# Kernel optimization log

Measured on AMD Instinct MI355X. Metric: run time of the kernel, lower is better.

## Reference

```python
import jax, jax.numpy as jnp
import numpy as np

DIM = 512
NUM_HEADS = 1
WS = 16
B, H, W = 2, WS * WS, 1


def _rel_pos_index(ws):
    # matches Attention.calculate_relative_position_index (no Swin offset -> negatives)
    coords = np.stack(np.meshgrid(np.arange(ws), np.arange(ws), indexing='ij'), 0).reshape(2, -1)
    rel = coords[:, :, None] - coords[:, None, :]          # [2, ws^2, ws^2]
    return rel.transpose(1, 2, 0).sum(-1)                  # [ws^2, ws^2] in [-(2ws-2), 2ws-2]

_NTAB = (2 * WS - 1) ** 2
# torch fancy indexing wraps negative indices; emulate with mod (values are in (-NTAB, NTAB))
_RPI = np.mod(_rel_pos_index(WS), _NTAB).reshape(-1)       # [ws^4]


def setup_inputs() -> dict:
    key = jax.random.key(0)
    ks = jax.random.split(key, 6)
    x = jax.random.normal(ks[0], (B, DIM, H, W), dtype=jnp.float32)
    qkv_w = jax.random.normal(ks[1], (3 * DIM, DIM), dtype=jnp.float32) * (DIM ** -0.5)
    qkv_b = jax.random.normal(ks[2], (3 * DIM,), dtype=jnp.float32) * 0.02
    proj_w = jax.random.normal(ks[3], (DIM, DIM), dtype=jnp.float32) * (DIM ** -0.5)
    proj_b = jax.random.normal(ks[4], (DIM,), dtype=jnp.float32) * 0.02
    rpb = jax.random.normal(ks[5], (_NTAB, NUM_HEADS), dtype=jnp.float32) * 0.02
    return {"x": x, "qkv_w": qkv_w, "qkv_b": qkv_b,
            "proj_w": proj_w, "proj_b": proj_b, "rpb": rpb}


def reference(x, qkv_w, qkv_b, proj_w, proj_b, rpb):
    b, c, h, w = x.shape                                   # [B, C, H, W=1]
    d = c // NUM_HEADS
    scale = d ** -0.5                                      # qk_scale=None -> (dim//nh)^-0.5
    # 1x1 conv == channel matmul
    qkv = jnp.einsum('bchw,oc->bohw', x, qkv_w) + qkv_b[None, :, None, None]
    qkv = qkv.reshape(b, 3, NUM_HEADS, d, h, w)
    q, k, v = qkv[:, 0], qkv[:, 1], qkv[:, 2]              # [B, nh, d, H, W]
    # matmul over last two dims: contracts W -> [B, nh, d, H, H]
    attn = jnp.einsum('bndhw,bndgw->bndhg', q, k) * scale
    idx = jnp.asarray(_RPI)
    bias = rpb[idx].reshape(h * w, h * w, -1).transpose(2, 0, 1)  # [nh, HW, HW] = [1, H, H]
    attn = jax.nn.softmax(attn + bias, axis=-1)
    out = jnp.einsum('bndhg,bndgw->bndhw', attn, v).sum(axis=1)   # sum over heads -> [B, d, H, W]
    out = jnp.einsum('bchw,oc->bohw', out, proj_w) + proj_b[None, :, None, None]
    return out
```

## Files before the change

### kernel.cpp

```cpp
#include <hip/hip_runtime.h>


#define TOK    256
#define KDIM   512
#define K8     64
#define LOG2E  1.4426950408889634f
#define SCALE  0.04419417382415922f

#define OFF_WQAH 0
#define OFF_WQAL 786432
#define OFF_XBH  1572864
#define OFF_XBL  1835008
#define OFF_WPAH 2097152
#define OFF_WPAL 2359296
#define OFF_AOBH 2621440
#define OFF_AOBL 2883584
#define OFF_QKVF 1572864

#define EXP2(x) __builtin_amdgcn_exp2f(x)

typedef __attribute__((ext_vector_type(8))) short short8_t;
typedef __attribute__((ext_vector_type(4))) float f32x4;

__device__ __forceinline__ unsigned short f2bf(float x) {
    unsigned int u = __float_as_uint(x);
    u += 0x7fffu + ((u >> 16) & 1u);
    return (unsigned short)(u >> 16);
}
__device__ __forceinline__ float bf2f(unsigned short h) {
    return __uint_as_float((unsigned int)h << 16);
}

__device__ __forceinline__ void cvt8(const float* v, unsigned short* hq,
                                     unsigned short* lq) {
#pragma unroll
    for (int j = 0; j < 8; ++j) {
        const unsigned short h = f2bf(v[j]);
        hq[j] = h;
        lq[j] = f2bf(v[j] - bf2f(h));
    }
}

__global__ __launch_bounds__(256)
void prep(const float* __restrict__ qkv_w, const float* __restrict__ x,
          const float* __restrict__ proj_w, unsigned short* __restrict__ U)
{
    const int id = blockIdx.x * 256 + threadIdx.x;
    alignas(16) unsigned short hq[8], lq[8];
    float v[8];

    if (id < 98304) {
        const int m = id >> 6, kc = id & 63;
        const float* s = qkv_w + (size_t)m * KDIM + kc * 8;
#pragma unroll
        for (int j = 0; j < 8; ++j) v[j] = s[j];
        cvt8(v, hq, lq);
        const size_t o = ((size_t)(m >> 4) * K8 + kc) * 128 + (size_t)(m & 15) * 8;
        *(uint4*)(U + OFF_WQAH + o) = *(const uint4*)hq;
        *(uint4*)(U + OFF_WQAL + o) = *(const uint4*)lq;
    } else if (id < 131072) {
        const int rid = id - 98304;
        const int n = rid & 255, kc = (rid >> 8) & 63, b = rid >> 14;
        const float* s = x + ((size_t)b * KDIM + kc * 8) * TOK + n;
#pragma unroll
        for (int j = 0; j < 8; ++j) v[j] = s[(size_t)j * TOK];
        cvt8(v, hq, lq);
        const size_t o = (((size_t)b * 16 + (n >> 4)) * K8 + kc) * 128
                         + (size_t)(n & 15) * 8;
        *(uint4*)(U + OFF_XBH + o) = *(const uint4*)hq;
        *(uint4*)(U + OFF_XBL + o) = *(const uint4*)lq;
    } else if (id < 163840) {
        const int rid = id - 131072;
        const int m = rid >> 6, kc = rid & 63;
        const float* s = proj_w + (size_t)m * KDIM + kc * 8;
#pragma unroll
        for (int j = 0; j < 8; ++j) v[j] = s[j];
        cvt8(v, hq, lq);
        const size_t o = ((size_t)(m >> 4) * K8 + kc) * 128 + (size_t)(m & 15) * 8;
        *(uint4*)(U + OFF_WPAH + o) = *(const uint4*)hq;
        *(uint4*)(U + OFF_WPAL + o) = *(const uint4*)lq;
    }
}

template<bool BIAS>
__global__ __launch_bounds__(64)
void gemm_frag(const unsigned short* __restrict__ Ah,
               const unsigned short* __restrict__ Al,
               const unsigned short* __restrict__ Bh,
               const unsigned short* __restrict__ Bl,
               const float* __restrict__ bias,
               float* __restrict__ Cout, int Mtot)
{
    const int t   = threadIdx.x;
    const int lr  = t & 15;
    const int lg  = t >> 4;
    const int mt0 = blockIdx.x * 2;
    const int nt0 = blockIdx.y * 4;
    const int b   = blockIdx.z;

    f32x4 acc[2][4];
#pragma unroll
    for (int mi = 0; mi < 2; ++mi)
#pragma unroll
        for (int ni = 0; ni < 4; ++ni)
            acc[mi][ni] = (f32x4){0.f, 0.f, 0.f, 0.f};

    short8_t ah[2][2], al[2][2], bh[2][4], bl[2][4];

#define LDF(S, P) do {                                                        \
        const int kc_ = (S) * 4 + lg;                                         \
        _Pragma("unroll")                                                     \
        for (int mi = 0; mi < 2; ++mi) {                                      \
            const size_t o_ = ((size_t)(mt0 + mi) * K8 + kc_) * 128           \
                              + (size_t)lr * 8;                               \
            ah[P][mi] = *(const short8_t*)(Ah + o_);                          \
            al[P][mi] = *(const short8_t*)(Al + o_);                          \
        }                                                                     \
        _Pragma("unroll")                                                     \
        for (int ni = 0; ni < 4; ++ni) {                                      \
            const size_t o_ = (((size_t)b * 16 + nt0 + ni) * K8 + kc_) * 128  \
                              + (size_t)lr * 8;                               \
            bh[P][ni] = *(const short8_t*)(Bh + o_);                          \
            bl[P][ni] = *(const short8_t*)(Bl + o_);                          \
        }                                                                     \
    } while (0)

    LDF(0, 0);
#pragma unroll
    for (int s = 0; s < 16; ++s) {
        const int p = s & 1;
        if (s + 1 < 16) LDF(s + 1, p ^ 1);
#pragma unroll
        for (int mi = 0; mi < 2; ++mi)
#pragma unroll
            for (int ni = 0; ni < 4; ++ni) {
                acc[mi][ni] = __builtin_amdgcn_mfma_f32_16x16x32_bf16(
                    ah[p][mi], bh[p][ni], acc[mi][ni], 0, 0, 0);
                acc[mi][ni] = __builtin_amdgcn_mfma_f32_16x16x32_bf16(
                    al[p][mi], bh[p][ni], acc[mi][ni], 0, 0, 0);
                acc[mi][ni] = __builtin_amdgcn_mfma_f32_16x16x32_bf16(
                    ah[p][mi], bl[p][ni], acc[mi][ni], 0, 0, 0);
            }
    }
#undef LDF

#pragma unroll
    for (int mi = 0; mi < 2; ++mi)
#pragma unroll
        for (int r = 0; r < 4; ++r) {
            const int row = (mt0 + mi) * 16 + lg * 4 + r;
            const float pb = BIAS ? bias[row] : 0.f;
#pragma unroll
            for (int ni = 0; ni < 4; ++ni) {
                const int col = (nt0 + ni) * 16 + lr;
                Cout[((size_t)b * Mtot + row) * TOK + col] = acc[mi][ni][r] + pb;
            }
        }
}

__global__ __launch_bounds__(256)
void attn_f32(const float* __restrict__ qkvf, const float* __restrict__ qkv_b,
              const float* __restrict__ rpb,
              unsigned short* __restrict__ aoh, unsigned short* __restrict__ aol)
{
    __shared__ float ks_[2][TOK];
    __shared__ float vs_[2][TOK];
    __shared__ float tab2[64];
    __shared__ float brow[31][258];
    __shared__ float lpart[2][TOK];
    __shared__ float apart[2][TOK];

    const int t  = threadIdx.x;
    const int b  = blockIdx.y;
    const int d0 = blockIdx.x * 2;
    const float* q0 = qkvf + (size_t)b * (1536 * TOK);

    if (t < 61) {
        const int rel = t - 30;
        tab2[t] = rpb[rel < 0 ? rel + 961 : rel] * LOG2E;
    }
    {
        const int sel = t >> 7;
        const int row = (t >> 6) & 1;
        const int g4  = (t & 63) * 4;
        const int o   = (sel ? 1024 : 512) + d0 + row;
        const float bb = qkv_b[o];
        float4 v = *(const float4*)(q0 + (size_t)o * TOK + g4);
        v.x += bb; v.y += bb; v.z += bb; v.w += bb;
        if (sel == 0) {
            const float s = SCALE * LOG2E;
            v.x *= s; v.y *= s; v.z *= s; v.w *= s;
            *(float4*)&ks_[row][g4] = v;
        } else {
            *(float4*)&vs_[row][g4] = v;
        }
    }
    __syncthreads();
    {
        const int rg = ((t >> 4) & 15) + (t & 15);
#pragma unroll 1
        for (int it = 0; it < 31; ++it)
            brow[it][t] = tab2[it - rg + 30];
    }
    __syncthreads();

    const int w   = t >> 6;
    const int dl  = w & 1;
    const int gh  = w >> 1;
    const int hl  = t & 63;
    const int qi  = ((hl & 15) << 2) | (hl >> 4);
    const int h0  = qi * 4;
    const int rh0 = (qi >> 2) + 4 * (qi & 3);

    float q[4];
    {
        const float bb = qkv_b[d0 + dl];
        const float4 x4 = *(const float4*)(q0 + (size_t)(d0 + dl) * TOK + h0);
        q[0] = x4.x + bb; q[1] = x4.y + bb; q[2] = x4.z + bb; q[3] = x4.w + bb;
    }

    float l[4]  = {0.f, 0.f, 0.f, 0.f};
    float am[4] = {0.f, 0.f, 0.f, 0.f};

    const int pbeg = gh * 128;
#pragma unroll 2
    for (int p = pbeg; p < pbeg + 128; p += 4) {
        const float4 k4 = *(const float4*)&ks_[dl][p];
        const float4 v4 = *(const float4*)&vs_[dl][p];
#pragma unroll
        for (int r = 0; r < 4; ++r) {
            const float2 b01 = *(const float2*)&brow[rh0 + r][p];
            const float2 b23 = *(const float2*)&brow[rh0 + r][p + 2];
            float e;
            e = EXP2(fmaf(q[r], k4.x, b01.x)); l[r] += e; am[r] = fmaf(e, v4.x, am[r]);
            e = EXP2(fmaf(q[r], k4.y, b01.y)); l[r] += e; am[r] = fmaf(e, v4.y, am[r]);
            e = EXP2(fmaf(q[r], k4.z, b23.x)); l[r] += e; am[r] = fmaf(e, v4.z, am[r]);
            e = EXP2(fmaf(q[r], k4.w, b23.y)); l[r] += e; am[r] = fmaf(e, v4.w, am[r]);
        }
    }

    if (gh == 1) {
        *(float4*)&lpart[dl][h0] = make_float4(l[0], l[1], l[2], l[3]);
        *(float4*)&apart[dl][h0] = make_float4(am[0], am[1], am[2], am[3]);
    }
    __syncthreads();
    if (gh == 0) {
        const float4 lo = *(const float4*)&lpart[dl][h0];
        const float4 ao = *(const float4*)&apart[dl][h0];
        float vals[4];
        vals[0] = (am[0] + ao.x) / (l[0] + lo.x);
        vals[1] = (am[1] + ao.y) / (l[1] + lo.y);
        vals[2] = (am[2] + ao.z) / (l[2] + lo.z);
        vals[3] = (am[3] + ao.w) / (l[3] + lo.w);
        const int d = d0 + dl;
        const size_t ob = (((size_t)b * 16 + (h0 >> 4)) * K8 + (d >> 3)) * 128
                          + (size_t)(h0 & 15) * 8 + (d & 7);
#pragma unroll
        for (int r = 0; r < 4; ++r) {
            const unsigned short hh = f2bf(vals[r]);
            aoh[ob + (size_t)r * 8] = hh;
            aol[ob + (size_t)r * 8] = f2bf(vals[r] - bf2f(hh));
        }
    }
}

extern "C" void kernel_launch(void* const* d_in, const int* in_sizes, int n_in,
                              void* d_out, int out_size, void* d_ws, size_t ws_size,
                              hipStream_t stream)
{
    const float* x      = (const float*)d_in[0];
    const float* qkv_w  = (const float*)d_in[1];
    const float* qkv_b  = (const float*)d_in[2];
    const float* proj_w = (const float*)d_in[3];
    const float* proj_b = (const float*)d_in[4];
    const float* rpb    = (const float*)d_in[5];
    float* out = (float*)d_out;

    unsigned short* U = (unsigned short*)d_ws;
    float* qkvf = (float*)d_ws + OFF_QKVF;

    prep<<<dim3(640), 256, 0, stream>>>(qkv_w, x, proj_w, U);

    gemm_frag<false><<<dim3(48, 4, 2), 64, 0, stream>>>(
        U + OFF_WQAH, U + OFF_WQAL, U + OFF_XBH, U + OFF_XBL,
        nullptr, qkvf, 1536);

    attn_f32<<<dim3(256, 2), 256, 0, stream>>>(qkvf, qkv_b, rpb,
                                               U + OFF_AOBH, U + OFF_AOBL);

    gemm_frag<true><<<dim3(16, 4, 2), 64, 0, stream>>>(
        U + OFF_WPAH, U + OFF_WPAL, U + OFF_AOBH, U + OFF_AOBL,
        proj_b, out, 512);
}
```

Measured before the change: 116.0 us.

## Split GEMM K-dimension across four waves with shared-memory reduction

Each GEMM block now runs four wavefronts that each handle a quarter of the K dimension. Their partial accumulators are summed through shared memory and written out as coalesced float4 stores. The projection GEMM also uses one M-tile per block, which doubles its block count. The goal is to shorten each wave's serial MFMA chain and give the small GEMMs more parallelism, at the cost of extra LDS traffic and a block-wide barrier.

```diff
diff --git a/kernel.cpp b/kernel.cpp
--- a/kernel.cpp
+++ b/kernel.cpp
@@ -82,8 +82,8 @@
     }
 }
 
-template<bool BIAS>
-__global__ __launch_bounds__(64)
+template<int MT, bool BIAS>
+__global__ __launch_bounds__(256)
 void gemm_frag(const unsigned short* __restrict__ Ah,
                const unsigned short* __restrict__ Al,
                const unsigned short* __restrict__ Bh,
@@ -91,26 +91,30 @@
                const float* __restrict__ bias,
                float* __restrict__ Cout, int Mtot)
 {
-    const int t   = threadIdx.x;
-    const int lr  = t & 15;
-    const int lg  = t >> 4;
-    const int mt0 = blockIdx.x * 2;
-    const int nt0 = blockIdx.y * 4;
-    const int b   = blockIdx.z;
-
-    f32x4 acc[2][4];
-#pragma unroll
-    for (int mi = 0; mi < 2; ++mi)
+    alignas(16) __shared__ float red[4][MT * 16][68];
+
+    const int t    = threadIdx.x;
+    const int w    = t >> 6;
+    const int lane = t & 63;
+    const int lr   = lane & 15;
+    const int lg   = lane >> 4;
+    const int mt0  = blockIdx.x * MT;
+    const int nt0  = blockIdx.y * 4;
+    const int b    = blockIdx.z;
+
+    f32x4 acc[MT][4];
+#pragma unroll
+    for (int mi = 0; mi < MT; ++mi)
 #pragma unroll
         for (int ni = 0; ni < 4; ++ni)
             acc[mi][ni] = (f32x4){0.f, 0.f, 0.f, 0.f};
 
-    short8_t ah[2][2], al[2][2], bh[2][4], bl[2][4];
+    short8_t ah[2][MT], al[2][MT], bh[2][4], bl[2][4];
 
 #define LDF(S, P) do {                                                        \
-        const int kc_ = (S) * 4 + lg;                                         \
+        const int kc_ = w * 16 + (S) * 4 + lg;                                \
         _Pragma("unroll")                                                     \
-        for (int mi = 0; mi < 2; ++mi) {                                      \
+        for (int mi = 0; mi < MT; ++mi) {                                     \
             const size_t o_ = ((size_t)(mt0 + mi) * K8 + kc_) * 128           \
                               + (size_t)lr * 8;                               \
             ah[P][mi] = *(const short8_t*)(Ah + o_);                          \
@@ -127,11 +131,11 @@
 
     LDF(0, 0);
 #pragma unroll
-    for (int s = 0; s < 16; ++s) {
+    for (int s = 0; s < 4; ++s) {
         const int p = s & 1;
-        if (s + 1 < 16) LDF(s + 1, p ^ 1);
-#pragma unroll
-        for (int mi = 0; mi < 2; ++mi)
+        if (s + 1 < 4) LDF(s + 1, p ^ 1);
+#pragma unroll
+        for (int mi = 0; mi < MT; ++mi)
 #pragma unroll
             for (int ni = 0; ni < 4; ++ni) {
                 acc[mi][ni] = __builtin_amdgcn_mfma_f32_16x16x32_bf16(
@@ -145,17 +149,33 @@
 #undef LDF
 
 #pragma unroll
-    for (int mi = 0; mi < 2; ++mi)
-#pragma unroll
-        for (int r = 0; r < 4; ++r) {
-            const int row = (mt0 + mi) * 16 + lg * 4 + r;
-            const float pb = BIAS ? bias[row] : 0.f;
-#pragma unroll
-            for (int ni = 0; ni < 4; ++ni) {
-                const int col = (nt0 + ni) * 16 + lr;
-                Cout[((size_t)b * Mtot + row) * TOK + col] = acc[mi][ni][r] + pb;
-            }
+    for (int mi = 0; mi < MT; ++mi)
+#pragma unroll
+        for (int ni = 0; ni < 4; ++ni)
+#pragma unroll
+            for (int r = 0; r < 4; ++r)
+                red[w][mi * 16 + lg * 4 + r][ni * 16 + lr] = acc[mi][ni][r];
+    __syncthreads();
+
+#pragma unroll
+    for (int it = 0; it < MT; ++it) {
+        const int rr = it * 16 + (t >> 4);
+        const int cc = (t & 15) * 4;
+        float4 v0 = *(const float4*)&red[0][rr][cc];
+        const float4 v1 = *(const float4*)&red[1][rr][cc];
+        const float4 v2 = *(const float4*)&red[2][rr][cc];
+        const float4 v3 = *(const float4*)&red[3][rr][cc];
+        v0.x += v1.x + v2.x + v3.x;
+        v0.y += v1.y + v2.y + v3.y;
+        v0.z += v1.z + v2.z + v3.z;
+        v0.w += v1.w + v2.w + v3.w;
+        const int grow = mt0 * 16 + rr;
+        if (BIAS) {
+            const float pb = bias[grow];
+            v0.x += pb; v0.y += pb; v0.z += pb; v0.w += pb;
         }
+        *(float4*)(Cout + ((size_t)b * Mtot + grow) * TOK + nt0 * 16 + cc) = v0;
+    }
 }
 
 __global__ __launch_bounds__(256)
@@ -281,14 +301,14 @@
 
     prep<<<dim3(640), 256, 0, stream>>>(qkv_w, x, proj_w, U);
 
-    gemm_frag<false><<<dim3(48, 4, 2), 64, 0, stream>>>(
+    gemm_frag<2, false><<<dim3(48, 4, 2), 256, 0, stream>>>(
         U + OFF_WQAH, U + OFF_WQAL, U + OFF_XBH, U + OFF_XBL,
         nullptr, qkvf, 1536);
 
     attn_f32<<<dim3(256, 2), 256, 0, stream>>>(qkvf, qkv_b, rpb,
                                                U + OFF_AOBH, U + OFF_AOBL);
 
-    gemm_frag<true><<<dim3(16, 4, 2), 64, 0, stream>>>(
+    gemm_frag<1, true><<<dim3(32, 4, 2), 256, 0, stream>>>(
         U + OFF_WPAH, U + OFF_WPAL, U + OFF_AOBH, U + OFF_AOBL,
         proj_b, out, 512);
 }
```

Measured after the change: 99.80 us (median of 2 runs). 13.9% less time.
